# Optimization experiments

Hardware: AMD Instinct MI355X
Metric: run time of the kernel (lower is better)

## Reference

```python
import jax, jax.numpy as jnp
import numpy as np

H, D, EPS = 4, 16, 1e-5
N_NODES, N_EDGES, F_IN, HID, N_GRAPHS, N_CLASSES = 100000, 1600000, 128, 64, 512, 10


def _bn(x, g, b, m, v):
    # BatchNorm1d in eval mode: running stats
    return (x - m) * jax.lax.rsqrt(v + EPS) * g + b


def _tconv(x, src, dst, wq, bq, wk, bk, wv, bv, ws, bs):
    # PyG TransformerConv: q from dst node, k/v from src node, scatter-softmax over dst,
    # scatter-add aggregation, concat heads, plus root (skip) linear. Dropout=eval (identity).
    N = x.shape[0]
    q = (x @ wq + bq).reshape(N, H, D)
    k = (x @ wk + bk).reshape(N, H, D)
    v = (x @ wv + bv).reshape(N, H, D)
    alpha = (q[dst] * k[src]).sum(-1) * np.float32(1.0 / np.sqrt(D))  # [E, H]
    amax = jax.ops.segment_max(alpha, dst, num_segments=N)            # [N, H]
    amax = jnp.where(jnp.isfinite(amax), amax, 0.0)
    ex = jnp.exp(alpha - amax[dst])
    denom = jax.ops.segment_sum(ex, dst, num_segments=N)
    attn = ex / (denom[dst] + 1e-16)                                  # [E, H]
    agg = jax.ops.segment_sum(attn[:, :, None] * v[src], dst, num_segments=N)  # [N, H, D]
    return agg.reshape(N, H * D) + x @ ws + bs


def setup_inputs() -> dict:
    key = jax.random.key(0)
    ks = list(jax.random.split(key, 40))
    def w(i, shape):
        return jax.random.normal(ks[i], shape, jnp.float32) * 0.05
    inp = {}
    inp['x'] = jax.random.normal(ks[0], (N_NODES, F_IN), jnp.float32)
    inp['edge_index'] = jax.random.randint(ks[1], (2, N_EDGES), 0, N_NODES, dtype=jnp.int32)
    inp['batch'] = jnp.sort(jax.random.randint(ks[2], (N_NODES,), 0, N_GRAPHS, dtype=jnp.int32))
    i = 3
    for p, fin in (('c1', F_IN), ('c2', HID)):
        for nm in ('wq', 'wk', 'wv', 'ws'):
            inp[p + '_' + nm] = w(i, (fin, HID)); i += 1
            inp[p + '_b' + nm[1]] = w(i, (HID,)); i += 1
    for p in ('bn1', 'bn2', 'clbn'):
        inp[p + '_g'] = jnp.ones((HID,), jnp.float32)
        inp[p + '_b'] = jnp.zeros((HID,), jnp.float32)
        inp[p + '_m'] = jnp.zeros((HID,), jnp.float32)
        inp[p + '_v'] = jnp.ones((HID,), jnp.float32)
    for nm, shp in (('p1_w', (HID, HID)), ('p2_w', (HID, HID)), ('cl1_w', (HID, HID)), ('cl2_w', (HID, N_CLASSES))):
        inp[nm] = w(i, shp); i += 1
    inp['p1_b'] = jnp.zeros((HID,), jnp.float32)
    inp['p2_b'] = jnp.zeros((HID,), jnp.float32)
    inp['cl1_b'] = jnp.zeros((HID,), jnp.float32)
    inp['cl2_b'] = jnp.zeros((N_CLASSES,), jnp.float32)
    return inp


def reference(x, edge_index, batch,
              c1_wq, c1_bq, c1_wk, c1_bk, c1_wv, c1_bv, c1_ws, c1_bs,
              bn1_g, bn1_b, bn1_m, bn1_v,
              c2_wq, c2_bq, c2_wk, c2_bk, c2_wv, c2_bv, c2_ws, c2_bs,
              bn2_g, bn2_b, bn2_m, bn2_v,
              p1_w, p1_b, p2_w, p2_b,
              cl1_w, cl1_b, clbn_g, clbn_b, clbn_m, clbn_v, cl2_w, cl2_b):
    src, dst = edge_index[0], edge_index[1]
    h = _tconv(x, src, dst, c1_wq, c1_bq, c1_wk, c1_bk, c1_wv, c1_bv, c1_ws, c1_bs)
    h = jax.nn.relu(_bn(h, bn1_g, bn1_b, bn1_m, bn1_v))
    h = _tconv(h, src, dst, c2_wq, c2_bq, c2_wk, c2_bk, c2_wv, c2_bv, c2_ws, c2_bs)
    h = jax.nn.relu(_bn(h, bn2_g, bn2_b, bn2_m, bn2_v))
    g = jax.ops.segment_max(h, batch, num_segments=N_GRAPHS)  # global_max_pool [G, HID]
    g = jnp.where(jnp.isfinite(g), g, 0.0)
    g = jax.nn.relu(g @ p1_w + p1_b) @ p2_w + p2_b
    g = jax.nn.relu(_bn(g @ cl1_w + cl1_b, clbn_g, clbn_b, clbn_m, clbn_v))
    logits = g @ cl2_w + cl2_b
    return jax.nn.log_softmax(logits, axis=1)
```

## Files before the change

### kernel.cpp

```cpp
#include <hip/hip_runtime.h>
#include <hip/hip_bf16.h>
#include <math.h>

constexpr int NN = 100000;
constexpr int EE = 1600000;
constexpr int GG = 512;
constexpr int MPAD = 100096;
constexpr int NBUCK = 782;
constexpr int EPB = 8192;
constexpr int CAP = 4096;

typedef __attribute__((ext_vector_type(8))) short short8;
typedef __attribute__((ext_vector_type(4))) float floatx4;

__device__ __forceinline__ unsigned short f2bf_rne(float f) {
    unsigned int u = __float_as_uint(f);
    u += 0x7fff + ((u >> 16) & 1);
    return (unsigned short)(u >> 16);
}

template<int C>
__device__ __forceinline__ float dppadd(float x) {
    int t = __builtin_amdgcn_update_dpp(0, __float_as_int(x), C, 0xf, 0xf, true);
    return x + __int_as_float(t);
}
__device__ __forceinline__ float qred4(float p) {
    p = dppadd<0xB1>(p);
    p = dppadd<0x4E>(p);
    return p;
}

__device__ __forceinline__ float dot4(uint2 kd, float q0, float q1, float q2, float q3) {
    float k0 = __uint_as_float(kd.x << 16);
    float k1 = __uint_as_float(kd.x & 0xffff0000u);
    float k2 = __uint_as_float(kd.y << 16);
    float k3 = __uint_as_float(kd.y & 0xffff0000u);
    return fmaf(k0, q0, fmaf(k1, q1, fmaf(k2, q2, k3 * q3)));
}

__global__ __launch_bounds__(512) void k_part(const int* __restrict__ src,
                                              const int* __restrict__ dst,
                                              int* __restrict__ bcur,
                                              unsigned int* __restrict__ ppair) {
    __shared__ int cnt[NBUCK];
    __shared__ int base[NBUCK];
    int tid = threadIdx.x;
    int e0 = blockIdx.x * EPB;
    for (int j = tid; j < NBUCK; j += 512) cnt[j] = 0;
    __syncthreads();
    int myd[16], myr[16];
    #pragma unroll
    for (int t = 0; t < 16; t++) {
        int i = e0 + t * 512 + tid;
        if (i < EE) {
            int d = dst[i];
            myd[t] = d;
            myr[t] = atomicAdd(&cnt[d >> 7], 1);
        } else myd[t] = -1;
    }
    __syncthreads();
    for (int j = tid; j < NBUCK; j += 512) base[j] = atomicAdd(&bcur[j], cnt[j]);
    __syncthreads();
    #pragma unroll
    for (int t = 0; t < 16; t++) {
        int i = e0 + t * 512 + tid;
        if (myd[t] >= 0) {
            int b = myd[t] >> 7;
            int pos = base[b] + myr[t];
            if (pos < CAP)
                ppair[(size_t)b * CAP + pos] =
                    ((unsigned int)src[i] << 7) | (unsigned int)(myd[t] & 127);
        }
    }
}

__global__ __launch_bounds__(256) void k_bucket(const unsigned int* __restrict__ ppair,
                                                const int* __restrict__ bcur,
                                                int* __restrict__ rowbeg,
                                                int* __restrict__ rowend,
                                                int* __restrict__ csr) {
    __shared__ int cnt[128];
    __shared__ int sa[128], sb[128];
    __shared__ int cur[128];
    int t = threadIdx.x;
    int b = blockIdx.x;
    int n = bcur[b]; if (n > CAP) n = CAP;
    int start = b * CAP;
    if (t < 128) cnt[t] = 0;
    __syncthreads();
    for (int i = t; i < n; i += 256)
        atomicAdd(&cnt[ppair[start + i] & 127], 1);
    __syncthreads();
    if (t < 128) sa[t] = cnt[t];
    __syncthreads();
    int* p = sa; int* q = sb;
    for (int off = 1; off < 128; off <<= 1) {
        if (t < 128) q[t] = (t >= off) ? (p[t] + p[t - off]) : p[t];
        __syncthreads();
        int* tmp = p; p = q; q = tmp;
    }
    if (t < 128) {
        int excl = (t == 0) ? 0 : p[t - 1];
        rowbeg[b * 128 + t] = start + excl;
        rowend[b * 128 + t] = start + p[t];
        cur[t] = start + excl;
    }
    __syncthreads();
    for (int i = t; i < n; i += 256) {
        unsigned int e = ppair[start + i];
        int pos = atomicAdd(&cur[e & 127], 1);
        csr[pos] = (int)(e >> 7);
    }
}

template<int K>
__global__ __launch_bounds__(256) void k_cvt_w(
    const float* __restrict__ Wq, const float* __restrict__ Bq,
    const float* __restrict__ Wk, const float* __restrict__ Bk,
    const float* __restrict__ Wv, const float* __restrict__ Bv,
    const float* __restrict__ Wsk, const float* __restrict__ Bsk,
    unsigned short* __restrict__ Bt, float* __restrict__ bias) {
    int idx = blockIdx.x * 256 + threadIdx.x;
    int col = idx / K, k = idx % K;
    float val;
    if (col < 64)        val = Wk[k * 64 + col];
    else if (col < 128)  val = Wv[k * 64 + (col - 64)];
    else if (col < 192)  val = Wq[k * 64 + (col - 128)];
    else                 val = Wsk[k * 64 + (col - 192)];
    Bt[col * K + k] = f2bf_rne(val);
    if (k == 0) {
        float bv;
        if (col < 64)        bv = Bk[col];
        else if (col < 128)  bv = Bv[col - 64];
        else if (col < 192)  bv = Bq[col - 128];
        else                 bv = Bsk[col - 192];
        bias[col] = bv;
    }
}

template<int K, bool AF32>
__global__ __launch_bounds__(256) void gemm_mfma(
    const void* __restrict__ Araw,
    const unsigned short* __restrict__ Bt,
    const float* __restrict__ bias,
    float* __restrict__ qs,
    unsigned short* __restrict__ kvu) {
    constexpr int SP = 72;
    __shared__ short As[128 * SP];
    __shared__ short Bs[128 * SP];
    int tid = threadIdx.x;
    int wave = tid >> 6, lane = tid & 63;
    int wm = wave >> 1, wn = wave & 1;
    int quad = lane >> 4, l16 = lane & 15;
    int rowBase = blockIdx.x * 128;
    int ct = blockIdx.y;

    floatx4 acc[4][4];
    #pragma unroll
    for (int i = 0; i < 4; i++)
        #pragma unroll
        for (int j = 0; j < 4; j++) acc[i][j] = (floatx4)0.f;

    for (int kc = 0; kc < K; kc += 64) {
        #pragma unroll
        for (int it = 0; it < 4; it++) {
            int flat = it * 256 + tid;
            int r = flat >> 3, c8 = (flat & 7) * 8;
            int ar = rowBase + r; if (ar >= NN) ar = NN - 1;
            short8 va;
            if constexpr (AF32) {
                const float* ap = (const float*)Araw + (size_t)ar * K + kc + c8;
                float4 u0 = *reinterpret_cast<const float4*>(ap);
                float4 u1 = *reinterpret_cast<const float4*>(ap + 4);
                va[0] = (short)f2bf_rne(u0.x); va[1] = (short)f2bf_rne(u0.y);
                va[2] = (short)f2bf_rne(u0.z); va[3] = (short)f2bf_rne(u0.w);
                va[4] = (short)f2bf_rne(u1.x); va[5] = (short)f2bf_rne(u1.y);
                va[6] = (short)f2bf_rne(u1.z); va[7] = (short)f2bf_rne(u1.w);
            } else {
                va = *reinterpret_cast<const short8*>(
                        (const unsigned short*)Araw + (size_t)ar * K + kc + c8);
            }
            *reinterpret_cast<short8*>(&As[r * SP + c8]) = va;
            short8 vb = *reinterpret_cast<const short8*>(Bt + (size_t)(ct * 128 + r) * K + kc + c8);
            *reinterpret_cast<short8*>(&Bs[r * SP + c8]) = vb;
        }
        __syncthreads();
        #pragma unroll
        for (int ks = 0; ks < 2; ks++) {
            short8 af[4], bf[4];
            #pragma unroll
            for (int i = 0; i < 4; i++)
                af[i] = *reinterpret_cast<const short8*>(&As[(wm * 64 + i * 16 + l16) * SP + ks * 32 + quad * 8]);
            #pragma unroll
            for (int j = 0; j < 4; j++)
                bf[j] = *reinterpret_cast<const short8*>(&Bs[(wn * 64 + j * 16 + l16) * SP + ks * 32 + quad * 8]);
            #pragma unroll
            for (int i = 0; i < 4; i++)
                #pragma unroll
                for (int j = 0; j < 4; j++)
                    acc[i][j] = __builtin_amdgcn_mfma_f32_16x16x32_bf16(af[i], bf[j], acc[i][j], 0, 0, 0);
        }
        __syncthreads();
    }

    float bj[4];
    #pragma unroll
    for (int j = 0; j < 4; j++) bj[j] = bias[ct * 128 + wn * 64 + j * 16 + l16];
    #pragma unroll
    for (int i = 0; i < 4; i++) {
        #pragma unroll
        for (int j = 0; j < 4; j++) {
            int col = wn * 64 + j * 16 + l16;
            #pragma unroll
            for (int r = 0; r < 4; r++) {
                int row = rowBase + wm * 64 + i * 16 + quad * 4 + r;
                if (row < NN) {
                    float val = acc[i][j][r] + bj[j];
                    if (ct == 1) qs[(size_t)row * 128 + col] = val;
                    else kvu[(size_t)row * 128 + col] = f2bf_rne(val);
                }
            }
        }
    }
}

__global__ __launch_bounds__(256) void attn_fused(
    const float* __restrict__ qs,
    const uint2* __restrict__ kvp,
    const int* __restrict__ rowbeg,
    const int* __restrict__ rowend,
    const int* __restrict__ csr,
    const float* __restrict__ bng, const float* __restrict__ bnb,
    const float* __restrict__ bnm, const float* __restrict__ bnv,
    uint2* __restrict__ h_out) {
    int wid = (blockIdx.x * 256 + threadIdx.x) >> 6;
    int lane = threadIdx.x & 63;
    if (wid >= NN) return;
    int g = lane >> 4, ql = lane & 15;
    const float* qrow = qs + (size_t)wid * 128;
    const float SC = 0.3606737602222409f;
    float4 q4 = reinterpret_cast<const float4*>(qrow)[ql];
    float q0 = q4.x * SC, q1 = q4.y * SC, q2 = q4.z * SC, q3 = q4.w * SC;
    int jb = rowbeg[wid], je = rowend[wid];
    float a0 = 0.f, a1 = 0.f, a2 = 0.f, a3 = 0.f, denom = 0.f;
    int j = jb;
    for (; j + 7 < je; j += 8) {
        int sA = csr[j + g];
        int sB = csr[j + 4 + g];
        const uint2* rA = kvp + (size_t)sA * 32;
        const uint2* rB = kvp + (size_t)sB * 32;
        uint2 kA = rA[ql], vA = rA[16 + ql];
        uint2 kB = rB[ql], vB = rB[16 + ql];
        float pA = qred4(dot4(kA, q0, q1, q2, q3));
        float pB = qred4(dot4(kB, q0, q1, q2, q3));
        float eA = exp2f(pA), eB = exp2f(pB);
        denom += eA + eB;
        a0 = fmaf(eA, __uint_as_float(vA.x << 16), a0);
        a1 = fmaf(eA, __uint_as_float(vA.x & 0xffff0000u), a1);
        a2 = fmaf(eA, __uint_as_float(vA.y << 16), a2);
        a3 = fmaf(eA, __uint_as_float(vA.y & 0xffff0000u), a3);
        a0 = fmaf(eB, __uint_as_float(vB.x << 16), a0);
        a1 = fmaf(eB, __uint_as_float(vB.x & 0xffff0000u), a1);
        a2 = fmaf(eB, __uint_as_float(vB.y << 16), a2);
        a3 = fmaf(eB, __uint_as_float(vB.y & 0xffff0000u), a3);
    }
    for (; j < je; j += 4) {
        int jj = j + g;
        bool valid = jj < je;
        int s = csr[valid ? jj : je - 1];
        const uint2* r = kvp + (size_t)s * 32;
        uint2 kd = r[ql], vd = r[16 + ql];
        float p = qred4(dot4(kd, q0, q1, q2, q3));
        float e = valid ? exp2f(p) : 0.f;
        denom += e;
        a0 = fmaf(e, __uint_as_float(vd.x << 16), a0);
        a1 = fmaf(e, __uint_as_float(vd.x & 0xffff0000u), a1);
        a2 = fmaf(e, __uint_as_float(vd.y << 16), a2);
        a3 = fmaf(e, __uint_as_float(vd.y & 0xffff0000u), a3);
    }
    a0 += __shfl_xor(a0, 16);  a0 += __shfl_xor(a0, 32);
    a1 += __shfl_xor(a1, 16);  a1 += __shfl_xor(a1, 32);
    a2 += __shfl_xor(a2, 16);  a2 += __shfl_xor(a2, 32);
    a3 += __shfl_xor(a3, 16);  a3 += __shfl_xor(a3, 32);
    denom += __shfl_xor(denom, 16);  denom += __shfl_xor(denom, 32);
    float inv = 1.f / (denom + 1e-16f);
    float4 s4 = reinterpret_cast<const float4*>(qrow + 64)[ql];
    float4 m4 = reinterpret_cast<const float4*>(bnm)[ql];
    float4 v4 = reinterpret_cast<const float4*>(bnv)[ql];
    float4 g4 = reinterpret_cast<const float4*>(bng)[ql];
    float4 b4 = reinterpret_cast<const float4*>(bnb)[ql];
    float o0 = a0 * inv + s4.x, o1 = a1 * inv + s4.y;
    float o2 = a2 * inv + s4.z, o3 = a3 * inv + s4.w;
    o0 = fmaxf((o0 - m4.x) * rsqrtf(v4.x + 1e-5f) * g4.x + b4.x, 0.f);
    o1 = fmaxf((o1 - m4.y) * rsqrtf(v4.y + 1e-5f) * g4.y + b4.y, 0.f);
    o2 = fmaxf((o2 - m4.z) * rsqrtf(v4.z + 1e-5f) * g4.z + b4.z, 0.f);
    o3 = fmaxf((o3 - m4.w) * rsqrtf(v4.w + 1e-5f) * g4.w + b4.w, 0.f);
    if (g == 0) {
        uint2 hw;
        hw.x = (unsigned int)f2bf_rne(o0) | ((unsigned int)f2bf_rne(o1) << 16);
        hw.y = (unsigned int)f2bf_rne(o2) | ((unsigned int)f2bf_rne(o3) << 16);
        h_out[(size_t)wid * 16 + ql] = hw;
    }
}

__global__ __launch_bounds__(256) void k_pool(const unsigned short* __restrict__ h,
                                              const int* __restrict__ batch,
                                              float* __restrict__ g0) {
    int f = threadIdx.x & 63;
    int sub = threadIdx.x >> 6;
    int n0 = blockIdx.x * 128;
    int nEnd = n0 + 128; if (nEnd > NN) nEnd = NN;
    int cur_g = -1; float cur_m = 0.f;
    for (int n = n0 + sub; n < nEnd; n += 4) {
        int bg = batch[n];
        float val = __uint_as_float((unsigned int)h[(size_t)n * 64 + f] << 16);
        if (bg != cur_g) {
            if (cur_g >= 0) atomicMax((int*)&g0[cur_g * 64 + f], __float_as_int(cur_m));
            cur_g = bg; cur_m = val;
        } else {
            cur_m = fmaxf(cur_m, val);
        }
    }
    if (cur_g >= 0) atomicMax((int*)&g0[cur_g * 64 + f], __float_as_int(cur_m));
}

__global__ __launch_bounds__(256) void k_mlp(
    const float* __restrict__ g0,
    const float* __restrict__ p1w, const float* __restrict__ p1b,
    const float* __restrict__ p2w, const float* __restrict__ p2b,
    const float* __restrict__ cl1w, const float* __restrict__ cl1b,
    const float* __restrict__ bg, const float* __restrict__ bb,
    const float* __restrict__ bm, const float* __restrict__ bv,
    const float* __restrict__ cl2w, const float* __restrict__ cl2b,
    float* __restrict__ outp) {
    __shared__ float w1[64 * 64], w2[64 * 64], w3[64 * 64], w4[64 * 10];
    __shared__ float sb1[64], sb2[64], sb3[64], sbn[4 * 64], sb4[10];
    int tid = threadIdx.x;
    for (int i = tid; i < 64 * 64; i += 256) { w1[i] = p1w[i]; w2[i] = p2w[i]; w3[i] = cl1w[i]; }
    for (int i = tid; i < 64 * 10; i += 256) w4[i] = cl2w[i];
    if (tid < 64) {
        sb1[tid] = p1b[tid]; sb2[tid] = p2b[tid]; sb3[tid] = cl1b[tid];
        sbn[tid] = bg[tid]; sbn[64 + tid] = bb[tid];
        sbn[128 + tid] = bm[tid]; sbn[192 + tid] = bv[tid];
    }
    if (tid < 10) sb4[tid] = cl2b[tid];
    __syncthreads();
    int lane = tid & 63, w = tid >> 6;
    int row = blockIdx.x * 4 + w;
    float x = g0[row * 64 + lane];
    if (!isfinite(x)) x = 0.f;
    float a = sb1[lane];
    for (int k = 0; k < 64; k++) a += __shfl(x, k) * w1[k * 64 + lane];
    x = fmaxf(a, 0.f);
    a = sb2[lane];
    for (int k = 0; k < 64; k++) a += __shfl(x, k) * w2[k * 64 + lane];
    x = a;
    a = sb3[lane];
    for (int k = 0; k < 64; k++) a += __shfl(x, k) * w3[k * 64 + lane];
    a = (a - sbn[128 + lane]) * rsqrtf(sbn[192 + lane] + 1e-5f) * sbn[lane] + sbn[64 + lane];
    x = fmaxf(a, 0.f);
    float lg[10];
    #pragma unroll
    for (int c = 0; c < 10; c++) {
        float p = x * w4[lane * 10 + c];
        p += __shfl_xor(p, 1);  p += __shfl_xor(p, 2);  p += __shfl_xor(p, 4);
        p += __shfl_xor(p, 8);  p += __shfl_xor(p, 16); p += __shfl_xor(p, 32);
        lg[c] = p + sb4[c];
    }
    float mx = lg[0];
    #pragma unroll
    for (int c = 1; c < 10; c++) mx = fmaxf(mx, lg[c]);
    float s = 0.f;
    #pragma unroll
    for (int c = 0; c < 10; c++) s += __expf(lg[c] - mx);
    float lse = mx + logf(s);
    float o = 0.f;
    #pragma unroll
    for (int c = 0; c < 10; c++) if (lane == c) o = lg[c];
    if (lane < 10) outp[row * 10 + lane] = o - lse;
}

extern "C" void kernel_launch(void* const* d_in, const int* in_sizes, int n_in,
                              void* d_out, int out_size, void* d_ws, size_t ws_size,
                              hipStream_t stream) {
    const float* x     = (const float*)d_in[0];
    const int*   ei    = (const int*)d_in[1];
    const int*   batch = (const int*)d_in[2];
    const float *c1_wq = (const float*)d_in[3],  *c1_bq = (const float*)d_in[4];
    const float *c1_wk = (const float*)d_in[5],  *c1_bk = (const float*)d_in[6];
    const float *c1_wv = (const float*)d_in[7],  *c1_bv = (const float*)d_in[8];
    const float *c1_ws = (const float*)d_in[9],  *c1_bs = (const float*)d_in[10];
    const float *c2_wq = (const float*)d_in[11], *c2_bq = (const float*)d_in[12];
    const float *c2_wk = (const float*)d_in[13], *c2_bk = (const float*)d_in[14];
    const float *c2_wv = (const float*)d_in[15], *c2_bv = (const float*)d_in[16];
    const float *c2_ws = (const float*)d_in[17], *c2_bs = (const float*)d_in[18];
    const float *bn1_g = (const float*)d_in[19], *bn1_b = (const float*)d_in[20];
    const float *bn1_m = (const float*)d_in[21], *bn1_v = (const float*)d_in[22];
    const float *bn2_g = (const float*)d_in[23], *bn2_b = (const float*)d_in[24];
    const float *bn2_m = (const float*)d_in[25], *bn2_v = (const float*)d_in[26];
    const float *clbn_g = (const float*)d_in[27], *clbn_b = (const float*)d_in[28];
    const float *clbn_m = (const float*)d_in[29], *clbn_v = (const float*)d_in[30];
    const float *p1_w = (const float*)d_in[31], *p2_w = (const float*)d_in[32];
    const float *cl1_w = (const float*)d_in[33], *cl2_w = (const float*)d_in[34];
    const float *p1_b = (const float*)d_in[35], *p2_b = (const float*)d_in[36];
    const float *cl1_b = (const float*)d_in[37], *cl2_b = (const float*)d_in[38];

    char* ws = (char*)d_ws;
    float*          qs     = (float*)(ws);
    unsigned int*   kv     = (unsigned int*)(ws + 51200000);
    unsigned short* hbuf   = (unsigned short*)(ws + 76800000);
    unsigned int*   ppair  = (unsigned int*)(ws + 89612288);
    int*            csr    = (int*)(ws + 102424576);
    int*            rowbeg = (int*)(ws + 115236864);
    int*            rowend = (int*)(ws + 115637248);
    int*            bcur   = (int*)(ws + 116037632);
    float*          g0     = (float*)(ws + 116040768);
    unsigned short* Bt1    = (unsigned short*)(ws + 116171840);
    float*          b1     = (float*)(ws + 116237376);
    unsigned short* Bt2    = (unsigned short*)(ws + 116238400);
    float*          b2     = (float*)(ws + 116271168);

    const int* srcIdx = ei;
    const int* dstIdx = ei + EE;

    hipMemsetAsync(bcur, 0, NBUCK * sizeof(int), stream);
    hipMemsetAsync(g0, 0, GG * 64 * sizeof(float), stream);

    constexpr int PBLK = (EE + EPB - 1) / EPB;
    k_part<<<PBLK, 512, 0, stream>>>(srcIdx, dstIdx, bcur, ppair);
    k_bucket<<<NBUCK, 256, 0, stream>>>(ppair, bcur, rowbeg, rowend, csr);

    k_cvt_w<128><<<128, 256, 0, stream>>>(c1_wq, c1_bq, c1_wk, c1_bk, c1_wv, c1_bv,
                                          c1_ws, c1_bs, Bt1, b1);
    k_cvt_w<64><<<64, 256, 0, stream>>>(c2_wq, c2_bq, c2_wk, c2_bk, c2_wv, c2_bv,
                                        c2_ws, c2_bs, Bt2, b2);

    {
        dim3 grid(MPAD / 128, 2);
        gemm_mfma<128, true><<<grid, 256, 0, stream>>>(x, Bt1, b1, qs, (unsigned short*)kv);
    }
    attn_fused<<<NN / 4, 256, 0, stream>>>(qs, (const uint2*)kv, rowbeg, rowend, csr,
                                           bn1_g, bn1_b, bn1_m, bn1_v, (uint2*)hbuf);

    {
        dim3 grid(MPAD / 128, 2);
        gemm_mfma<64, false><<<grid, 256, 0, stream>>>(hbuf, Bt2, b2, qs, (unsigned short*)kv);
    }
    attn_fused<<<NN / 4, 256, 0, stream>>>(qs, (const uint2*)kv, rowbeg, rowend, csr,
                                           bn2_g, bn2_b, bn2_m, bn2_v, (uint2*)hbuf);

    k_pool<<<(NN + 127) / 128, 256, 0, stream>>>(hbuf, batch, g0);
    k_mlp<<<GG / 4, 256, 0, stream>>>(g0, p1_w, p1_b, p2_w, p2_b, cl1_w, cl1_b,
                                      clbn_g, clbn_b, clbn_m, clbn_v, cl2_w, cl2_b,
                                      (float*)d_out);
}
```

Before: 422.6 us.

## Store q/skip projections in bf16, read GEMM B directly, merge weight conversion

The q and skip-linear outputs of the projection GEMM are now written as bf16 instead of fp32, which halves their write traffic and the per-node reads in the attention kernel. The GEMM no longer stages the weight tile in shared memory; each wave loads its B fragments straight from global memory, where the small weight matrix should stay cached. The two weight-conversion launches and the pooling-buffer memset are folded into one kernel. The cost is lower precision on queries and the skip path, plus possibly less efficient global B loads.

```diff
diff --git a/kernel.cpp b/kernel.cpp
--- a/kernel.cpp
+++ b/kernel.cpp
@@ -18,6 +18,8 @@
     u += 0x7fff + ((u >> 16) & 1);
     return (unsigned short)(u >> 16);
 }
+__device__ __forceinline__ float bf_lo(unsigned int u) { return __uint_as_float(u << 16); }
+__device__ __forceinline__ float bf_hi(unsigned int u) { return __uint_as_float(u & 0xffff0000u); }
 
 template<int C>
 __device__ __forceinline__ float dppadd(float x) {
@@ -31,11 +33,8 @@
 }
 
 __device__ __forceinline__ float dot4(uint2 kd, float q0, float q1, float q2, float q3) {
-    float k0 = __uint_as_float(kd.x << 16);
-    float k1 = __uint_as_float(kd.x & 0xffff0000u);
-    float k2 = __uint_as_float(kd.y << 16);
-    float k3 = __uint_as_float(kd.y & 0xffff0000u);
-    return fmaf(k0, q0, fmaf(k1, q1, fmaf(k2, q2, k3 * q3)));
+    return fmaf(bf_lo(kd.x), q0, fmaf(bf_hi(kd.x), q1,
+           fmaf(bf_lo(kd.y), q2, bf_hi(kd.y) * q3)));
 }
 
 __global__ __launch_bounds__(512) void k_part(const int* __restrict__ src,
@@ -113,28 +112,54 @@
     }
 }
 
-template<int K>
-__global__ __launch_bounds__(256) void k_cvt_w(
-    const float* __restrict__ Wq, const float* __restrict__ Bq,
-    const float* __restrict__ Wk, const float* __restrict__ Bk,
-    const float* __restrict__ Wv, const float* __restrict__ Bv,
-    const float* __restrict__ Wsk, const float* __restrict__ Bsk,
-    unsigned short* __restrict__ Bt, float* __restrict__ bias) {
-    int idx = blockIdx.x * 256 + threadIdx.x;
-    int col = idx / K, k = idx % K;
-    float val;
-    if (col < 64)        val = Wk[k * 64 + col];
-    else if (col < 128)  val = Wv[k * 64 + (col - 64)];
-    else if (col < 192)  val = Wq[k * 64 + (col - 128)];
-    else                 val = Wsk[k * 64 + (col - 192)];
-    Bt[col * K + k] = f2bf_rne(val);
-    if (k == 0) {
-        float bv;
-        if (col < 64)        bv = Bk[col];
-        else if (col < 128)  bv = Bv[col - 64];
-        else if (col < 192)  bv = Bq[col - 128];
-        else                 bv = Bsk[col - 192];
-        bias[col] = bv;
+__global__ __launch_bounds__(256) void k_cvt_all(
+    const float* __restrict__ w1q, const float* __restrict__ b1q,
+    const float* __restrict__ w1k, const float* __restrict__ b1k,
+    const float* __restrict__ w1v, const float* __restrict__ b1v,
+    const float* __restrict__ w1s, const float* __restrict__ b1s,
+    const float* __restrict__ w2q, const float* __restrict__ b2q,
+    const float* __restrict__ w2k, const float* __restrict__ b2k,
+    const float* __restrict__ w2v, const float* __restrict__ b2v,
+    const float* __restrict__ w2s, const float* __restrict__ b2s,
+    unsigned short* __restrict__ Bt1, float* __restrict__ bias1,
+    unsigned short* __restrict__ Bt2, float* __restrict__ bias2,
+    float* __restrict__ g0) {
+    int b = blockIdx.x, tid = threadIdx.x;
+    if (b < 128) {
+        g0[b * 256 + tid] = 0.f;
+        int idx = b * 256 + tid;
+        int col = idx >> 7, k = idx & 127;
+        float val;
+        if (col < 64)        val = w1k[k * 64 + col];
+        else if (col < 128)  val = w1v[k * 64 + (col - 64)];
+        else if (col < 192)  val = w1q[k * 64 + (col - 128)];
+        else                 val = w1s[k * 64 + (col - 192)];
+        Bt1[col * 128 + k] = f2bf_rne(val);
+        if (k == 0) {
+            float bv;
+            if (col < 64)        bv = b1k[col];
+            else if (col < 128)  bv = b1v[col - 64];
+            else if (col < 192)  bv = b1q[col - 128];
+            else                 bv = b1s[col - 192];
+            bias1[col] = bv;
+        }
+    } else {
+        int idx = (b - 128) * 256 + tid;
+        int col = idx >> 6, k = idx & 63;
+        float val;
+        if (col < 64)        val = w2k[k * 64 + col];
+        else if (col < 128)  val = w2v[k * 64 + (col - 64)];
+        else if (col < 192)  val = w2q[k * 64 + (col - 128)];
+        else                 val = w2s[k * 64 + (col - 192)];
+        Bt2[col * 64 + k] = f2bf_rne(val);
+        if (k == 0) {
+            float bv;
+            if (col < 64)        bv = b2k[col];
+            else if (col < 128)  bv = b2v[col - 64];
+            else if (col < 192)  bv = b2q[col - 128];
+            else                 bv = b2s[col - 192];
+            bias2[col] = bv;
+        }
     }
 }
 
@@ -143,17 +168,21 @@
     const void* __restrict__ Araw,
     const unsigned short* __restrict__ Bt,
     const float* __restrict__ bias,
-    float* __restrict__ qs,
-    unsigned short* __restrict__ kvu) {
+    unsigned short* __restrict__ out0,
+    unsigned short* __restrict__ out1) {
     constexpr int SP = 72;
     __shared__ short As[128 * SP];
-    __shared__ short Bs[128 * SP];
     int tid = threadIdx.x;
     int wave = tid >> 6, lane = tid & 63;
     int wm = wave >> 1, wn = wave & 1;
     int quad = lane >> 4, l16 = lane & 15;
     int rowBase = blockIdx.x * 128;
     int ct = blockIdx.y;
+
+    const unsigned short* bRow[4];
+    #pragma unroll
+    for (int j = 0; j < 4; j++)
+        bRow[j] = Bt + (size_t)(ct * 128 + wn * 64 + j * 16 + l16) * K + quad * 8;
 
     floatx4 acc[4][4];
     #pragma unroll
@@ -181,8 +210,6 @@
                         (const unsigned short*)Araw + (size_t)ar * K + kc + c8);
             }
             *reinterpret_cast<short8*>(&As[r * SP + c8]) = va;
-            short8 vb = *reinterpret_cast<const short8*>(Bt + (size_t)(ct * 128 + r) * K + kc + c8);
-            *reinterpret_cast<short8*>(&Bs[r * SP + c8]) = vb;
         }
         __syncthreads();
         #pragma unroll
@@ -193,7 +220,7 @@
                 af[i] = *reinterpret_cast<const short8*>(&As[(wm * 64 + i * 16 + l16) * SP + ks * 32 + quad * 8]);
             #pragma unroll
             for (int j = 0; j < 4; j++)
-                bf[j] = *reinterpret_cast<const short8*>(&Bs[(wn * 64 + j * 16 + l16) * SP + ks * 32 + quad * 8]);
+                bf[j] = *reinterpret_cast<const short8*>(bRow[j] + kc + ks * 32);
             #pragma unroll
             for (int i = 0; i < 4; i++)
                 #pragma unroll
@@ -203,6 +230,7 @@
         __syncthreads();
     }
 
+    unsigned short* outp = ct ? out1 : out0;
     float bj[4];
     #pragma unroll
     for (int j = 0; j < 4; j++) bj[j] = bias[ct * 128 + wn * 64 + j * 16 + l16];
@@ -214,18 +242,15 @@
             #pragma unroll
             for (int r = 0; r < 4; r++) {
                 int row = rowBase + wm * 64 + i * 16 + quad * 4 + r;
-                if (row < NN) {
-                    float val = acc[i][j][r] + bj[j];
-                    if (ct == 1) qs[(size_t)row * 128 + col] = val;
-                    else kvu[(size_t)row * 128 + col] = f2bf_rne(val);
-                }
+                if (row < NN)
+                    outp[(size_t)row * 128 + col] = f2bf_rne(acc[i][j][r] + bj[j]);
             }
         }
     }
 }
 
 __global__ __launch_bounds__(256) void attn_fused(
-    const float* __restrict__ qs,
+    const unsigned short* __restrict__ qsb,
     const uint2* __restrict__ kvp,
     const int* __restrict__ rowbeg,
     const int* __restrict__ rowend,
@@ -237,10 +262,11 @@
     int lane = threadIdx.x & 63;
     if (wid >= NN) return;
     int g = lane >> 4, ql = lane & 15;
-    const float* qrow = qs + (size_t)wid * 128;
+    const uint2* qrow = reinterpret_cast<const uint2*>(qsb + (size_t)wid * 128);
     const float SC = 0.3606737602222409f;
-    float4 q4 = reinterpret_cast<const float4*>(qrow)[ql];
-    float q0 = q4.x * SC, q1 = q4.y * SC, q2 = q4.z * SC, q3 = q4.w * SC;
+    uint2 qd = qrow[ql];
+    float q0 = bf_lo(qd.x) * SC, q1 = bf_hi(qd.x) * SC;
+    float q2 = bf_lo(qd.y) * SC, q3 = bf_hi(qd.y) * SC;
     int jb = rowbeg[wid], je = rowend[wid];
     float a0 = 0.f, a1 = 0.f, a2 = 0.f, a3 = 0.f, denom = 0.f;
     int j = jb;
@@ -255,14 +281,14 @@
         float pB = qred4(dot4(kB, q0, q1, q2, q3));
         float eA = exp2f(pA), eB = exp2f(pB);
         denom += eA + eB;
-        a0 = fmaf(eA, __uint_as_float(vA.x << 16), a0);
-        a1 = fmaf(eA, __uint_as_float(vA.x & 0xffff0000u), a1);
-        a2 = fmaf(eA, __uint_as_float(vA.y << 16), a2);
-        a3 = fmaf(eA, __uint_as_float(vA.y & 0xffff0000u), a3);
-        a0 = fmaf(eB, __uint_as_float(vB.x << 16), a0);
-        a1 = fmaf(eB, __uint_as_float(vB.x & 0xffff0000u), a1);
-        a2 = fmaf(eB, __uint_as_float(vB.y << 16), a2);
-        a3 = fmaf(eB, __uint_as_float(vB.y & 0xffff0000u), a3);
+        a0 = fmaf(eA, bf_lo(vA.x), a0);
+        a1 = fmaf(eA, bf_hi(vA.x), a1);
+        a2 = fmaf(eA, bf_lo(vA.y), a2);
+        a3 = fmaf(eA, bf_hi(vA.y), a3);
+        a0 = fmaf(eB, bf_lo(vB.x), a0);
+        a1 = fmaf(eB, bf_hi(vB.x), a1);
+        a2 = fmaf(eB, bf_lo(vB.y), a2);
+        a3 = fmaf(eB, bf_hi(vB.y), a3);
     }
     for (; j < je; j += 4) {
         int jj = j + g;
@@ -273,10 +299,10 @@
         float p = qred4(dot4(kd, q0, q1, q2, q3));
         float e = valid ? exp2f(p) : 0.f;
         denom += e;
-        a0 = fmaf(e, __uint_as_float(vd.x << 16), a0);
-        a1 = fmaf(e, __uint_as_float(vd.x & 0xffff0000u), a1);
-        a2 = fmaf(e, __uint_as_float(vd.y << 16), a2);
-        a3 = fmaf(e, __uint_as_float(vd.y & 0xffff0000u), a3);
+        a0 = fmaf(e, bf_lo(vd.x), a0);
+        a1 = fmaf(e, bf_hi(vd.x), a1);
+        a2 = fmaf(e, bf_lo(vd.y), a2);
+        a3 = fmaf(e, bf_hi(vd.y), a3);
     }
     a0 += __shfl_xor(a0, 16);  a0 += __shfl_xor(a0, 32);
     a1 += __shfl_xor(a1, 16);  a1 += __shfl_xor(a1, 32);
@@ -284,13 +310,13 @@
     a3 += __shfl_xor(a3, 16);  a3 += __shfl_xor(a3, 32);
     denom += __shfl_xor(denom, 16);  denom += __shfl_xor(denom, 32);
     float inv = 1.f / (denom + 1e-16f);
-    float4 s4 = reinterpret_cast<const float4*>(qrow + 64)[ql];
+    uint2 sd = qrow[16 + ql];
     float4 m4 = reinterpret_cast<const float4*>(bnm)[ql];
     float4 v4 = reinterpret_cast<const float4*>(bnv)[ql];
     float4 g4 = reinterpret_cast<const float4*>(bng)[ql];
     float4 b4 = reinterpret_cast<const float4*>(bnb)[ql];
-    float o0 = a0 * inv + s4.x, o1 = a1 * inv + s4.y;
-    float o2 = a2 * inv + s4.z, o3 = a3 * inv + s4.w;
+    float o0 = a0 * inv + bf_lo(sd.x), o1 = a1 * inv + bf_hi(sd.x);
+    float o2 = a2 * inv + bf_lo(sd.y), o3 = a3 * inv + bf_hi(sd.y);
     o0 = fmaxf((o0 - m4.x) * rsqrtf(v4.x + 1e-5f) * g4.x + b4.x, 0.f);
     o1 = fmaxf((o1 - m4.y) * rsqrtf(v4.y + 1e-5f) * g4.y + b4.y, 0.f);
     o2 = fmaxf((o2 - m4.z) * rsqrtf(v4.z + 1e-5f) * g4.z + b4.z, 0.f);
@@ -406,47 +432,46 @@
     const float *cl1_b = (const float*)d_in[37], *cl2_b = (const float*)d_in[38];
 
     char* ws = (char*)d_ws;
-    float*          qs     = (float*)(ws);
-    unsigned int*   kv     = (unsigned int*)(ws + 51200000);
-    unsigned short* hbuf   = (unsigned short*)(ws + 76800000);
-    unsigned int*   ppair  = (unsigned int*)(ws + 89612288);
-    int*            csr    = (int*)(ws + 102424576);
-    int*            rowbeg = (int*)(ws + 115236864);
-    int*            rowend = (int*)(ws + 115637248);
-    int*            bcur   = (int*)(ws + 116037632);
-    float*          g0     = (float*)(ws + 116040768);
-    unsigned short* Bt1    = (unsigned short*)(ws + 116171840);
-    float*          b1     = (float*)(ws + 116237376);
-    unsigned short* Bt2    = (unsigned short*)(ws + 116238400);
-    float*          b2     = (float*)(ws + 116271168);
+    unsigned short* kv     = (unsigned short*)(ws);
+    unsigned short* qsb    = (unsigned short*)(ws + 25600000);
+    unsigned short* hbuf   = (unsigned short*)(ws + 51200000);
+    unsigned int*   ppair  = (unsigned int*)(ws + 64012288);
+    int*            csr    = (int*)(ws + 76824576);
+    int*            rowbeg = (int*)(ws + 89636864);
+    int*            rowend = (int*)(ws + 90037248);
+    int*            bcur   = (int*)(ws + 90437632);
+    float*          g0     = (float*)(ws + 90440768);
+    unsigned short* Bt1    = (unsigned short*)(ws + 90571840);
+    float*          b1     = (float*)(ws + 90637376);
+    unsigned short* Bt2    = (unsigned short*)(ws + 90638400);
+    float*          b2     = (float*)(ws + 90671168);
 
     const int* srcIdx = ei;
     const int* dstIdx = ei + EE;
 
     hipMemsetAsync(bcur, 0, NBUCK * sizeof(int), stream);
-    hipMemsetAsync(g0, 0, GG * 64 * sizeof(float), stream);
+
+    k_cvt_all<<<192, 256, 0, stream>>>(c1_wq, c1_bq, c1_wk, c1_bk, c1_wv, c1_bv,
+                                       c1_ws, c1_bs,
+                                       c2_wq, c2_bq, c2_wk, c2_bk, c2_wv, c2_bv,
+                                       c2_ws, c2_bs, Bt1, b1, Bt2, b2, g0);
 
     constexpr int PBLK = (EE + EPB - 1) / EPB;
     k_part<<<PBLK, 512, 0, stream>>>(srcIdx, dstIdx, bcur, ppair);
     k_bucket<<<NBUCK, 256, 0, stream>>>(ppair, bcur, rowbeg, rowend, csr);
 
-    k_cvt_w<128><<<128, 256, 0, stream>>>(c1_wq, c1_bq, c1_wk, c1_bk, c1_wv, c1_bv,
-                                          c1_ws, c1_bs, Bt1, b1);
-    k_cvt_w<64><<<64, 256, 0, stream>>>(c2_wq, c2_bq, c2_wk, c2_bk, c2_wv, c2_bv,
-                                        c2_ws, c2_bs, Bt2, b2);
-
     {
         dim3 grid(MPAD / 128, 2);
-        gemm_mfma<128, true><<<grid, 256, 0, stream>>>(x, Bt1, b1, qs, (unsigned short*)kv);
-    }
-    attn_fused<<<NN / 4, 256, 0, stream>>>(qs, (const uint2*)kv, rowbeg, rowend, csr,
+        gemm_mfma<128, true><<<grid, 256, 0, stream>>>(x, Bt1, b1, kv, qsb);
+    }
+    attn_fused<<<NN / 4, 256, 0, stream>>>(qsb, (const uint2*)kv, rowbeg, rowend, csr,
                                            bn1_g, bn1_b, bn1_m, bn1_v, (uint2*)hbuf);
 
     {
         dim3 grid(MPAD / 128, 2);
-        gemm_mfma<64, false><<<grid, 256, 0, stream>>>(hbuf, Bt2, b2, qs, (unsigned short*)kv);
-    }
-    attn_fused<<<NN / 4, 256, 0, stream>>>(qs, (const uint2*)kv, rowbeg, rowend, csr,
+        gemm_mfma<64, false><<<grid, 256, 0, stream>>>(hbuf, Bt2, b2, kv, qsb);
+    }
+    attn_fused<<<NN / 4, 256, 0, stream>>>(qsb, (const uint2*)kv, rowbeg, rowend, csr,
                                            bn2_g, bn2_b, bn2_m, bn2_v, (uint2*)hbuf);
 
     k_pool<<<(NN + 127) / 128, 256, 0, stream>>>(hbuf, batch, g0);
```

After: 411.3 us. 1.03x faster.
